# Optimization experiments

Hardware: AMD Instinct MI355X
Metric: run time of the kernel (lower is better)

Reference implementation:

```python
import jax, jax.numpy as jnp
import numpy as np

D_MODEL = 768
HEADS = 12
D_K = D_MODEL // HEADS
NEG = -1e9


def setup_inputs() -> dict:
    key = jax.random.key(0)
    ks = jax.random.split(key, 7)
    B, S, D = 4, 2048, D_MODEL
    scale = 1.0 / np.sqrt(D)
    q = jax.random.normal(ks[0], (B, S, D), dtype=jnp.float32)
    k = jax.random.normal(ks[1], (B, S, D), dtype=jnp.float32)
    v = jax.random.normal(ks[2], (B, S, D), dtype=jnp.float32)
    # causal mask, broadcastable over batch and heads; mask==0 -> -1e9
    mask = jnp.tril(jnp.ones((1, 1, S, S), dtype=jnp.int32))
    W_q = jax.random.normal(ks[3], (D, D), dtype=jnp.float32) * scale
    W_k = jax.random.normal(ks[4], (D, D), dtype=jnp.float32) * scale
    W_v = jax.random.normal(ks[5], (D, D), dtype=jnp.float32) * scale
    W_o = jax.random.normal(ks[6], (D, D), dtype=jnp.float32) * scale
    return {"q": q, "k": k, "v": v, "mask": mask,
            "W_q": W_q, "W_k": W_k, "W_v": W_v, "W_o": W_o}


def reference(q, k, v, mask, W_q, W_k, W_v, W_o):
    B, S, D = q.shape
    # nn.Linear(bias=False): y = x @ W.T
    query = (q @ W_q.T).reshape(B, S, HEADS, D_K).transpose(0, 2, 1, 3)  # [B,H,S,dk]
    key_ = (k @ W_k.T).reshape(B, S, HEADS, D_K).transpose(0, 2, 1, 3)
    value = (v @ W_v.T).reshape(B, S, HEADS, D_K).transpose(0, 2, 1, 3)
    scores = jnp.einsum('bhqd,bhkd->bhqk', query, key_) / jnp.sqrt(
        jnp.asarray(D_K, dtype=query.dtype))
    scores = jnp.where(mask == 0, jnp.asarray(NEG, dtype=scores.dtype), scores)
    attn = jax.nn.softmax(scores, axis=-1)
    # dropout rate = 0.0 (inference / eval mode): identity
    x = jnp.einsum('bhqk,bhkd->bhqd', attn, value)  # [B,H,S,dk]
    x = x.transpose(0, 2, 1, 3).reshape(B, S, D)
    return x @ W_o.T
```

## Files before the change

kernel.cpp:

```cpp
#include <hip/hip_runtime.h>


typedef _Float16 f16x8 __attribute__((ext_vector_type(8)));
typedef _Float16 f16x4 __attribute__((ext_vector_type(4)));
typedef float floatx4 __attribute__((ext_vector_type(4)));

#define MFMA16(a, b, c) __builtin_amdgcn_mfma_f32_16x16x32_f16((a), (b), (c), 0, 0, 0)

static constexpr int B_ = 4;
static constexpr int S_ = 2048;
static constexpr int D_ = 768;
static constexpr int H_ = 12;
static constexpr int DK = 64;

__device__ __forceinline__ f16x8 cvt8(float4 a, float4 b) {
  f16x8 h;
  h[0] = (_Float16)a.x; h[1] = (_Float16)a.y;
  h[2] = (_Float16)a.z; h[3] = (_Float16)a.w;
  h[4] = (_Float16)b.x; h[5] = (_Float16)b.y;
  h[6] = (_Float16)b.z; h[7] = (_Float16)b.w;
  return h;
}

__device__ __forceinline__ void dma16(const _Float16* g, _Float16* l) {
  __builtin_amdgcn_global_load_lds(
      (const __attribute__((address_space(1))) unsigned int*)g,
      (__attribute__((address_space(3))) unsigned int*)l, 16, 0, 0);
}

struct CvtArgs {
  const float* src[7];
  _Float16* dst[7];
  int end[7];
  int nseg;
};

__global__ __launch_bounds__(256) void cvt_f32_f16(CvtArgs a) {
  int b = blockIdx.x;
  int s = 0;
  while (s < a.nseg - 1 && b >= a.end[s]) ++s;
  int local = b - (s ? a.end[s - 1] : 0);
  const int tid = threadIdx.x;
  const float4* p = (const float4*)(a.src[s] + (size_t)local * 2048) + tid * 2;
  float4 x0 = p[0], x1 = p[1];
  *(f16x8*)(a.dst[s] + (size_t)local * 2048 + tid * 8) = cvt8(x0, x1);
}

static constexpr int PAN = 128 * 32;

struct QkvPtrs {
  const void* a[3];
  const void* w[3];
};

template <int MODE, bool SCALE>
__device__ __forceinline__ void gemm_core64(const _Float16* __restrict__ A,
                                            const _Float16* __restrict__ Bm,
                                            void* __restrict__ Cv,
                                            _Float16* As, _Float16* Bs,
                                            int m0, int n0, int N, int K) {
  const int tid = threadIdx.x;
  const int wave = tid >> 6, lane = tid & 63;
  const int l15 = lane & 15, quad = lane >> 4;
  const int wm = (wave >> 1) * 64, wn = (wave & 1) * 64;
  const int lr = lane >> 2;
  const int lc = (lane & 3) * 8;
  const int wb = wave * 16;

  floatx4 acc[4][4] = {};

  for (int k0 = 0; k0 < K; k0 += 64) {
    {
      const _Float16* g = A + (size_t)(m0 + wb + lr) * K + k0 + lc;
      dma16(g, As + wb * 32);
      dma16(g + 32, As + PAN + wb * 32);
      const _Float16* g2 = g + (size_t)64 * K;
      dma16(g2, As + (64 + wb) * 32);
      dma16(g2 + 32, As + PAN + (64 + wb) * 32);
    }
    {
      const _Float16* g = Bm + (size_t)(n0 + wb + lr) * K + k0 + lc;
      dma16(g, Bs + wb * 32);
      dma16(g + 32, Bs + PAN + wb * 32);
      const _Float16* g2 = g + (size_t)64 * K;
      dma16(g2, Bs + (64 + wb) * 32);
      dma16(g2 + 32, Bs + PAN + (64 + wb) * 32);
    }
    __syncthreads();

#pragma unroll
    for (int p = 0; p < 2; ++p) {
      f16x8 af[4], bf[4];
#pragma unroll
      for (int t = 0; t < 4; ++t)
        af[t] = *(const f16x8*)(As + p * PAN + (wm + t * 16 + l15) * 32 +
                                quad * 8);
#pragma unroll
      for (int t = 0; t < 4; ++t)
        bf[t] = *(const f16x8*)(Bs + p * PAN + (wn + t * 16 + l15) * 32 +
                                quad * 8);
#pragma unroll
      for (int mt = 0; mt < 4; ++mt)
#pragma unroll
        for (int nt = 0; nt < 4; ++nt)
          acc[mt][nt] = MFMA16(af[mt], bf[nt], acc[mt][nt]);
    }
    __syncthreads();
  }

  if constexpr (MODE == 2) {
#pragma unroll
    for (int mt = 0; mt < 4; ++mt)
#pragma unroll
      for (int nt = 0; nt < 4; ++nt) {
        int row = m0 + wm + mt * 16 + quad * 4;
        int col = n0 + wn + nt * 16 + l15;
        int b = row >> 11, s = row & 2047;
        int h = col >> 6, d = col & 63;
        f16x4 v4;
#pragma unroll
        for (int r = 0; r < 4; ++r) v4[r] = (_Float16)acc[mt][nt][r];
        *(f16x4*)((_Float16*)Cv + ((size_t)(b * H_ + h) * DK + d) * S_ + s) =
            v4;
      }
  } else {
#pragma unroll
    for (int mt = 0; mt < 4; ++mt)
#pragma unroll
      for (int nt = 0; nt < 4; ++nt)
#pragma unroll
        for (int r = 0; r < 4; ++r) {
          int row = m0 + wm + mt * 16 + quad * 4 + r;
          int col = n0 + wn + nt * 16 + l15;
          float val = acc[mt][nt][r];
          if constexpr (SCALE) val *= 0.125f;
          if constexpr (MODE == 0) {
            ((float*)Cv)[(size_t)row * N + col] = val;
          } else {
            int b = row >> 11, s = row & 2047;
            int h = col >> 6, d = col & 63;
            ((_Float16*)Cv)[((size_t)(b * H_ + h) * S_ + s) * DK + d] =
                (_Float16)val;
          }
        }
  }
}

__global__ __launch_bounds__(256) void qkv_gemm64(QkvPtrs P, _Float16* Qh,
                                                  _Float16* Kh, _Float16* Vt) {
  __shared__ _Float16 As[2 * PAN];
  __shared__ _Float16 Bs[2 * PAN];
  const int linear =
      blockIdx.x + gridDim.x * (blockIdx.y + gridDim.y * blockIdx.z);
  const int xcd = linear & 7;
  const int idx = linear >> 3;
  const int z = idx / 48;
  const int r = idx % 48;
  const int mp = xcd * 8 + (r / 6);
  const int n = r % 6;
  const int m0 = mp * 128, n0 = n * 128;
  if (z == 0) {
    gemm_core64<1, true>((const _Float16*)P.a[0], (const _Float16*)P.w[0], Qh,
                         As, Bs, m0, n0, D_, D_);
  } else if (z == 1) {
    gemm_core64<1, false>((const _Float16*)P.a[1], (const _Float16*)P.w[1], Kh,
                          As, Bs, m0, n0, D_, D_);
  } else {
    gemm_core64<2, false>((const _Float16*)P.a[2], (const _Float16*)P.w[2], Vt,
                          As, Bs, m0, n0, D_, D_);
  }
}

static constexpr int PAN_A = 64 * 32;
static constexpr int PAN_B = 128 * 32;

__global__ __launch_bounds__(256) void gemm_o64(const _Float16* __restrict__ A,
                                                const _Float16* __restrict__ W,
                                                float* __restrict__ C) {
  __shared__ _Float16 As[2 * PAN_A];
  __shared__ _Float16 Bs[2 * PAN_B];
  constexpr int K = 768, N = 768;

  const int linear = blockIdx.x + gridDim.x * blockIdx.y;
  const int xcd = linear & 7;
  const int idx = linear >> 3;
  const int mp = xcd * 16 + idx / 6;
  const int n = idx % 6;
  const int m0 = mp * 64, n0 = n * 128;

  const int tid = threadIdx.x;
  const int wave = tid >> 6, lane = tid & 63;
  const int l15 = lane & 15, quad = lane >> 4;
  const int wm = (wave >> 1) * 32, wn = (wave & 1) * 64;
  const int lr = lane >> 2, lc = (lane & 3) * 8;

  floatx4 acc[2][4] = {};

  for (int k0 = 0; k0 < K; k0 += 64) {
#pragma unroll
    for (int p = 0; p < 2; ++p) {
      const _Float16* g =
          A + (size_t)(m0 + wave * 16 + lr) * K + k0 + p * 32 + lc;
      dma16(g, As + p * PAN_A + wave * 16 * 32);
    }
#pragma unroll
    for (int p = 0; p < 2; ++p)
#pragma unroll
      for (int q = 0; q < 2; ++q) {
        const _Float16* g =
            W + (size_t)(n0 + wave * 32 + q * 16 + lr) * K + k0 + p * 32 + lc;
        dma16(g, Bs + p * PAN_B + (wave * 32 + q * 16) * 32);
      }
    __syncthreads();

#pragma unroll
    for (int p = 0; p < 2; ++p) {
      f16x8 af[2], bf[4];
#pragma unroll
      for (int t = 0; t < 2; ++t)
        af[t] = *(const f16x8*)(As + p * PAN_A + (wm + t * 16 + l15) * 32 +
                                quad * 8);
#pragma unroll
      for (int t = 0; t < 4; ++t)
        bf[t] = *(const f16x8*)(Bs + p * PAN_B + (wn + t * 16 + l15) * 32 +
                                quad * 8);
#pragma unroll
      for (int mt = 0; mt < 2; ++mt)
#pragma unroll
        for (int nt = 0; nt < 4; ++nt)
          acc[mt][nt] = MFMA16(af[mt], bf[nt], acc[mt][nt]);
    }
    __syncthreads();
  }

#pragma unroll
  for (int mt = 0; mt < 2; ++mt)
#pragma unroll
    for (int nt = 0; nt < 4; ++nt)
#pragma unroll
      for (int r = 0; r < 4; ++r) {
        int row = m0 + wm + mt * 16 + quad * 4 + r;
        int col = n0 + wn + nt * 16 + l15;
        C[(size_t)row * N + col] = acc[mt][nt][r];
      }
}

__global__ __launch_bounds__(256, 4) void flash_attn(
    const _Float16* __restrict__ Qh, const _Float16* __restrict__ Kh,
    const _Float16* __restrict__ Vt, _Float16* __restrict__ Oh) {
  __shared__ _Float16 Ks[64 * 72];
  __shared__ _Float16 Vts[64 * 72];
  __shared__ _Float16 Ps[4][16 * 36];

  const int tid = threadIdx.x;
  const int wave = tid >> 6, lane = tid & 63;
  const int l15 = lane & 15, quad = lane >> 4;

  const int linear = blockIdx.x + gridDim.x * blockIdx.y;
  const int xcd = linear & 7;
  const int seq = linear >> 3;
  const int bh = xcd * 6 + (seq >> 4);
  const int xp = seq & 15;
  const int b = bh / H_, h = bh % H_;
  const size_t base = (size_t)bh * S_ * DK;
  const size_t basev = (size_t)bh * DK * S_;

  const int srow = tid >> 2;
  const int sc0 = (tid & 3) * 16;

  for (int c = 0; c < 2; ++c) {
    const int qt = c ? xp : 31 - xp;
    const int q0 = qt * 64;
    const int qrow = q0 + wave * 16 + l15;
    f16x8 qf0 = *(const f16x8*)(Qh + base + (size_t)qrow * DK + quad * 8);
    f16x8 qf1 = *(const f16x8*)(Qh + base + (size_t)qrow * DK + 32 + quad * 8);

    floatx4 o_acc[4] = {};
    float plsum[4] = {0.f, 0.f, 0.f, 0.f};

    const _Float16* ks = Kh + base + (size_t)srow * DK + sc0;
    const _Float16* vs = Vt + basev + (size_t)srow * S_ + sc0;
    f16x8 pk0 = *(const f16x8*)ks;
    f16x8 pk1 = *(const f16x8*)(ks + 8);
    f16x8 pv0 = *(const f16x8*)vs;
    f16x8 pv1 = *(const f16x8*)(vs + 8);

    for (int j = 0; j <= qt; ++j) {
      __syncthreads();
      *(f16x8*)(Ks + srow * 72 + sc0) = pk0;
      *(f16x8*)(Ks + srow * 72 + sc0 + 8) = pk1;
      *(f16x8*)(Vts + srow * 72 + sc0) = pv0;
      *(f16x8*)(Vts + srow * 72 + sc0 + 8) = pv1;
      __syncthreads();

      if (j < qt) {
        const _Float16* kn =
            Kh + base + (size_t)((j + 1) * 64 + srow) * DK + sc0;
        const _Float16* vn =
            Vt + basev + (size_t)srow * S_ + (j + 1) * 64 + sc0;
        pk0 = *(const f16x8*)kn;
        pk1 = *(const f16x8*)(kn + 8);
        pv0 = *(const f16x8*)vn;
        pv1 = *(const f16x8*)(vn + 8);
      }

      floatx4 s_acc[4] = {};
#pragma unroll
      for (int t = 0; t < 4; ++t) {
        f16x8 kf0 = *(const f16x8*)(Ks + (t * 16 + l15) * 72 + quad * 8);
        f16x8 kf1 = *(const f16x8*)(Ks + (t * 16 + l15) * 72 + 32 + quad * 8);
        s_acc[t] = MFMA16(qf0, kf0, s_acc[t]);
        s_acc[t] = MFMA16(qf1, kf1, s_acc[t]);
      }

      const bool diag = (j == qt);
      const int j0 = j * 64;
      float p[4][4];
#pragma unroll
      for (int t = 0; t < 4; ++t)
#pragma unroll
        for (int r = 0; r < 4; ++r) {
          float s = s_acc[t][r];
          if (diag) {
            int rg = q0 + wave * 16 + quad * 4 + r;
            int cg = j0 + t * 16 + l15;
            if (cg > rg) s = -1e30f;
          }
          float e = __expf(s);
          p[t][r] = e;
          plsum[r] += e;
        }

#pragma unroll
      for (int t = 0; t < 2; ++t)
#pragma unroll
        for (int r = 0; r < 4; ++r)
          Ps[wave][(quad * 4 + r) * 36 + t * 16 + l15] = (_Float16)p[t][r];
      f16x8 pf0 = *(const f16x8*)(Ps[wave] + l15 * 36 + quad * 8);
#pragma unroll
      for (int t = 0; t < 4; ++t) {
        f16x8 vf0 = *(const f16x8*)(Vts + (t * 16 + l15) * 72 + quad * 8);
        o_acc[t] = MFMA16(pf0, vf0, o_acc[t]);
      }
#pragma unroll
      for (int t = 2; t < 4; ++t)
#pragma unroll
        for (int r = 0; r < 4; ++r)
          Ps[wave][(quad * 4 + r) * 36 + (t - 2) * 16 + l15] =
              (_Float16)p[t][r];
      f16x8 pf1 = *(const f16x8*)(Ps[wave] + l15 * 36 + quad * 8);
#pragma unroll
      for (int t = 0; t < 4; ++t) {
        f16x8 vf1 = *(const f16x8*)(Vts + (t * 16 + l15) * 72 + 32 + quad * 8);
        o_acc[t] = MFMA16(pf1, vf1, o_acc[t]);
      }
    }

#pragma unroll
    for (int r = 0; r < 4; ++r) {
      float l = plsum[r];
      l += __shfl_xor(l, 1);
      l += __shfl_xor(l, 2);
      l += __shfl_xor(l, 4);
      l += __shfl_xor(l, 8);
      float inv = 1.0f / l;
      int row = q0 + wave * 16 + quad * 4 + r;
#pragma unroll
      for (int t = 0; t < 4; ++t) {
        float val = o_acc[t][r] * inv;
        Oh[((size_t)(b * S_ + row)) * D_ + h * DK + t * 16 + l15] =
            (_Float16)val;
      }
    }
  }
}

template <int MODE, bool SCALE>
__global__ __launch_bounds__(256) void gemm128(const float* __restrict__ Av,
                                               const float* __restrict__ Bv,
                                               void* __restrict__ Cv, int M,
                                               int N, int K) {
  __shared__ _Float16 As[128 * 40];
  __shared__ _Float16 Bs[128 * 40];

  const int tid = threadIdx.x;
  const int wave = tid >> 6, lane = tid & 63;
  const int l15 = lane & 15, quad = lane >> 4;
  const int wm = (wave >> 1) * 64, wn = (wave & 1) * 64;
  const int m0 = blockIdx.y * 128, n0 = blockIdx.x * 128;
  const int srow = tid >> 1, scol = (tid & 1) * 16;

  floatx4 acc[4][4] = {};

  for (int k0 = 0; k0 < K; k0 += 32) {
    {
      const float4* p =
          (const float4*)(Av + (size_t)(m0 + srow) * K + k0 + scol);
      float4 x0 = p[0], x1 = p[1], x2 = p[2], x3 = p[3];
      *(f16x8*)(As + srow * 40 + scol) = cvt8(x0, x1);
      *(f16x8*)(As + srow * 40 + scol + 8) = cvt8(x2, x3);
    }
    {
      const float4* p =
          (const float4*)(Bv + (size_t)(n0 + srow) * K + k0 + scol);
      float4 x0 = p[0], x1 = p[1], x2 = p[2], x3 = p[3];
      *(f16x8*)(Bs + srow * 40 + scol) = cvt8(x0, x1);
      *(f16x8*)(Bs + srow * 40 + scol + 8) = cvt8(x2, x3);
    }
    __syncthreads();

    f16x8 af[4], bf[4];
#pragma unroll
    for (int t = 0; t < 4; ++t)
      af[t] = *(const f16x8*)(As + (wm + t * 16 + l15) * 40 + quad * 8);
#pragma unroll
    for (int t = 0; t < 4; ++t)
      bf[t] = *(const f16x8*)(Bs + (wn + t * 16 + l15) * 40 + quad * 8);
#pragma unroll
    for (int mt = 0; mt < 4; ++mt)
#pragma unroll
      for (int nt = 0; nt < 4; ++nt)
        acc[mt][nt] = MFMA16(af[mt], bf[nt], acc[mt][nt]);
    __syncthreads();
  }

#pragma unroll
  for (int mt = 0; mt < 4; ++mt)
#pragma unroll
    for (int nt = 0; nt < 4; ++nt)
#pragma unroll
      for (int r = 0; r < 4; ++r) {
        int row = m0 + wm + mt * 16 + quad * 4 + r;
        int col = n0 + wn + nt * 16 + l15;
        float val = acc[mt][nt][r];
        if constexpr (SCALE) val *= 0.125f;
        if constexpr (MODE == 0) {
          ((float*)Cv)[(size_t)row * N + col] = val;
        } else if constexpr (MODE == 1) {
          int b = row >> 11, s = row & 2047;
          int h = col >> 6, d = col & 63;
          ((_Float16*)Cv)[((size_t)(b * H_ + h) * S_ + s) * DK + d] =
              (_Float16)val;
        } else {
          int b = col >> 11, s = col & 2047;
          int h = row >> 6, d = row & 63;
          ((_Float16*)Cv)[((size_t)(b * H_ + h) * DK + d) * S_ + s] =
              (_Float16)val;
        }
      }
}

__global__ __launch_bounds__(256) void gemm_out_f32w(
    const _Float16* __restrict__ A, const float* __restrict__ Bv,
    float* __restrict__ C) {
  __shared__ _Float16 As[128 * 40];
  __shared__ _Float16 Bs[128 * 40];
  constexpr int K = 768, N = 768;

  const int tid = threadIdx.x;
  const int wave = tid >> 6, lane = tid & 63;
  const int l15 = lane & 15, quad = lane >> 4;
  const int wm = (wave >> 1) * 64, wn = (wave & 1) * 64;
  const int m0 = blockIdx.y * 128, n0 = blockIdx.x * 128;
  const int srow = tid >> 1, scol = (tid & 1) * 16;

  floatx4 acc[4][4] = {};

  for (int k0 = 0; k0 < K; k0 += 32) {
    {
      const f16x8* p = (const f16x8*)(A + (size_t)(m0 + srow) * K + k0 + scol);
      *(f16x8*)(As + srow * 40 + scol) = p[0];
      *(f16x8*)(As + srow * 40 + scol + 8) = p[1];
    }
    {
      const float4* p =
          (const float4*)(Bv + (size_t)(n0 + srow) * K + k0 + scol);
      float4 x0 = p[0], x1 = p[1], x2 = p[2], x3 = p[3];
      *(f16x8*)(Bs + srow * 40 + scol) = cvt8(x0, x1);
      *(f16x8*)(Bs + srow * 40 + scol + 8) = cvt8(x2, x3);
    }
    __syncthreads();

    f16x8 af[4], bf[4];
#pragma unroll
    for (int t = 0; t < 4; ++t)
      af[t] = *(const f16x8*)(As + (wm + t * 16 + l15) * 40 + quad * 8);
#pragma unroll
    for (int t = 0; t < 4; ++t)
      bf[t] = *(const f16x8*)(Bs + (wn + t * 16 + l15) * 40 + quad * 8);
#pragma unroll
    for (int mt = 0; mt < 4; ++mt)
#pragma unroll
      for (int nt = 0; nt < 4; ++nt)
        acc[mt][nt] = MFMA16(af[mt], bf[nt], acc[mt][nt]);
    __syncthreads();
  }

#pragma unroll
  for (int mt = 0; mt < 4; ++mt)
#pragma unroll
    for (int nt = 0; nt < 4; ++nt)
#pragma unroll
      for (int r = 0; r < 4; ++r) {
        int row = m0 + wm + mt * 16 + quad * 4 + r;
        int col = n0 + wn + nt * 16 + l15;
        C[(size_t)row * N + col] = acc[mt][nt][r];
      }
}

extern "C" void kernel_launch(void* const* d_in, const int* in_sizes, int n_in,
                              void* d_out, int out_size, void* d_ws,
                              size_t ws_size, hipStream_t stream) {
  const float* q = (const float*)d_in[0];
  const float* k = (const float*)d_in[1];
  const float* v = (const float*)d_in[2];
  const float* Wq = (const float*)d_in[4];
  const float* Wk = (const float*)d_in[5];
  const float* Wv = (const float*)d_in[6];
  const float* Wo = (const float*)d_in[7];
  float* out = (float*)d_out;

  const size_t E = (size_t)B_ * H_ * S_ * DK;
  const size_t EW = (size_t)D_ * D_;
  _Float16* Qh = (_Float16*)d_ws;
  _Float16* Kh = Qh + E;
  _Float16* Vt = Kh + E;
  _Float16* Oh = Vt + E;

  const int M = B_ * S_;
  dim3 blk(256);
  dim3 qg(D_ / 128, M / 128, 3);
  dim3 og(D_ / 128, M / 64);
  dim3 pg(D_ / 128, M / 128);
  dim3 fg(16, B_ * H_);

  const size_t need_full = (7 * E + 4 * EW) * 2;

  if (ws_size >= need_full) {
    _Float16* qf = Oh + E;
    _Float16* kf = qf + E;
    _Float16* vf = kf + E;
    _Float16* wqf = vf + E;
    _Float16* wkf = wqf + EW;
    _Float16* wvf = wkf + EW;
    _Float16* wof = wvf + EW;
    CvtArgs ca;
    ca.src[0] = q;  ca.dst[0] = qf;
    ca.src[1] = k;  ca.dst[1] = kf;
    ca.src[2] = v;  ca.dst[2] = vf;
    ca.src[3] = Wq; ca.dst[3] = wqf;
    ca.src[4] = Wk; ca.dst[4] = wkf;
    ca.src[5] = Wv; ca.dst[5] = wvf;
    ca.src[6] = Wo; ca.dst[6] = wof;
    int ends[7] = {3072, 6144, 9216, 9504, 9792, 10080, 10368};
    for (int i = 0; i < 7; ++i) ca.end[i] = ends[i];
    ca.nseg = 7;
    cvt_f32_f16<<<10368, blk, 0, stream>>>(ca);
    QkvPtrs P;
    P.a[0] = qf; P.a[1] = kf; P.a[2] = vf;
    P.w[0] = wqf; P.w[1] = wkf; P.w[2] = wvf;
    qkv_gemm64<<<qg, blk, 0, stream>>>(P, Qh, Kh, Vt);
    flash_attn<<<fg, blk, 0, stream>>>(Qh, Kh, Vt, Oh);
    gemm_o64<<<og, blk, 0, stream>>>(Oh, wof, out);
  } else {
    gemm128<1, true><<<pg, blk, 0, stream>>>(q, Wq, Qh, M, D_, D_);
    gemm128<1, false><<<pg, blk, 0, stream>>>(k, Wk, Kh, M, D_, D_);
    gemm128<2, false><<<dim3(M / 128, D_ / 128), blk, 0, stream>>>(
        Wv, v, Vt, D_, M, D_);
    flash_attn<<<fg, blk, 0, stream>>>(Qh, Kh, Vt, Oh);
    gemm_out_f32w<<<pg, blk, 0, stream>>>(Oh, Wo, out);
  }
}
```

Baseline: 245.5 us.

## Rework flash attention to 32x32 MFMA tiles with key-split waves

The attention kernel moves from 16x16x32 MFMA tiles to 32x32x16 tiles. The four waves are reorganised into two row halves times two key halves, and each loop iteration stages a 128-key K/V tile. The two key-half partial outputs and row sums are combined through shared memory at the end. The goal is fewer MFMA issues and fewer LDS fragment reads per FLOP. In exchange the kernel uses more registers and LDS, is limited to 3 blocks per SM, adds extra syncs, and causal masking leaves some key-half waves idle.

```diff
diff --git a/kernel.cpp b/kernel.cpp
--- a/kernel.cpp
+++ b/kernel.cpp
@@ -4,8 +4,10 @@
 typedef _Float16 f16x8 __attribute__((ext_vector_type(8)));
 typedef _Float16 f16x4 __attribute__((ext_vector_type(4)));
 typedef float floatx4 __attribute__((ext_vector_type(4)));
+typedef float floatx16 __attribute__((ext_vector_type(16)));
 
 #define MFMA16(a, b, c) __builtin_amdgcn_mfma_f32_16x16x32_f16((a), (b), (c), 0, 0, 0)
+#define MFMA32(a, b, c) __builtin_amdgcn_mfma_f32_32x32x16_f16((a), (b), (c), 0, 0, 0)
 
 static constexpr int B_ = 4;
 static constexpr int S_ = 2048;
@@ -245,16 +247,17 @@
       }
 }
 
-__global__ __launch_bounds__(256, 4) void flash_attn(
+__global__ __launch_bounds__(256, 3) void flash_attn(
     const _Float16* __restrict__ Qh, const _Float16* __restrict__ Kh,
     const _Float16* __restrict__ Vt, _Float16* __restrict__ Oh) {
-  __shared__ _Float16 Ks[64 * 72];
-  __shared__ _Float16 Vts[64 * 72];
-  __shared__ _Float16 Ps[4][16 * 36];
+  __shared__ _Float16 Ks[128 * 72];
+  __shared__ _Float16 Vts[64 * 136];
+  __shared__ _Float16 Ps[4][32 * 36];
 
   const int tid = threadIdx.x;
   const int wave = tid >> 6, lane = tid & 63;
-  const int l15 = lane & 15, quad = lane >> 4;
+  const int l31 = lane & 31, sub = lane >> 5;
+  const int rowhalf = wave & 1, keyhalf = wave >> 1;
 
   const int linear = blockIdx.x + gridDim.x * blockIdx.y;
   const int xcd = linear & 7;
@@ -266,112 +269,148 @@
   const size_t basev = (size_t)bh * DK * S_;
 
   const int srow = tid >> 2;
-  const int sc0 = (tid & 3) * 16;
+  const int scol = (tid & 3) * 16;
+  const int vcol = (tid & 3) * 32;
 
   for (int c = 0; c < 2; ++c) {
     const int qt = c ? xp : 31 - xp;
     const int q0 = qt * 64;
-    const int qrow = q0 + wave * 16 + l15;
-    f16x8 qf0 = *(const f16x8*)(Qh + base + (size_t)qrow * DK + quad * 8);
-    f16x8 qf1 = *(const f16x8*)(Qh + base + (size_t)qrow * DK + 32 + quad * 8);
-
-    floatx4 o_acc[4] = {};
-    float plsum[4] = {0.f, 0.f, 0.f, 0.f};
-
-    const _Float16* ks = Kh + base + (size_t)srow * DK + sc0;
-    const _Float16* vs = Vt + basev + (size_t)srow * S_ + sc0;
-    f16x8 pk0 = *(const f16x8*)ks;
-    f16x8 pk1 = *(const f16x8*)(ks + 8);
-    f16x8 pv0 = *(const f16x8*)vs;
-    f16x8 pv1 = *(const f16x8*)(vs + 8);
-
-    for (int j = 0; j <= qt; ++j) {
+    const int nt = qt + 1;
+    const int iters = (nt + 1) >> 1;
+    const int rbase = q0 + rowhalf * 32;
+
+    f16x8 qf[4];
+#pragma unroll
+    for (int ks = 0; ks < 4; ++ks)
+      qf[ks] = *(const f16x8*)(Qh + base + (size_t)(rbase + l31) * DK +
+                               ks * 16 + sub * 8);
+
+    floatx16 o0 = {}, o1 = {};
+    float plsum[16] = {};
+
+    f16x8 pk[4], pv[4];
+    {
+      const _Float16* kp = Kh + base + (size_t)srow * DK + scol;
+      pk[0] = *(const f16x8*)kp;
+      pk[1] = *(const f16x8*)(kp + 8);
+      const _Float16* kp2 = kp + (size_t)64 * DK;
+      pk[2] = *(const f16x8*)kp2;
+      pk[3] = *(const f16x8*)(kp2 + 8);
+      const _Float16* vp = Vt + basev + (size_t)srow * S_ + vcol;
+#pragma unroll
+      for (int j = 0; j < 4; ++j) pv[j] = *(const f16x8*)(vp + j * 8);
+    }
+
+    for (int i = 0; i < iters; ++i) {
       __syncthreads();
-      *(f16x8*)(Ks + srow * 72 + sc0) = pk0;
-      *(f16x8*)(Ks + srow * 72 + sc0 + 8) = pk1;
-      *(f16x8*)(Vts + srow * 72 + sc0) = pv0;
-      *(f16x8*)(Vts + srow * 72 + sc0 + 8) = pv1;
+      *(f16x8*)(Ks + srow * 72 + scol) = pk[0];
+      *(f16x8*)(Ks + srow * 72 + scol + 8) = pk[1];
+      *(f16x8*)(Ks + (64 + srow) * 72 + scol) = pk[2];
+      *(f16x8*)(Ks + (64 + srow) * 72 + scol + 8) = pk[3];
+#pragma unroll
+      for (int j = 0; j < 4; ++j)
+        *(f16x8*)(Vts + srow * 136 + vcol + j * 8) = pv[j];
       __syncthreads();
 
-      if (j < qt) {
-        const _Float16* kn =
-            Kh + base + (size_t)((j + 1) * 64 + srow) * DK + sc0;
-        const _Float16* vn =
-            Vt + basev + (size_t)srow * S_ + (j + 1) * 64 + sc0;
-        pk0 = *(const f16x8*)kn;
-        pk1 = *(const f16x8*)(kn + 8);
-        pv0 = *(const f16x8*)vn;
-        pv1 = *(const f16x8*)(vn + 8);
-      }
-
-      floatx4 s_acc[4] = {};
-#pragma unroll
-      for (int t = 0; t < 4; ++t) {
-        f16x8 kf0 = *(const f16x8*)(Ks + (t * 16 + l15) * 72 + quad * 8);
-        f16x8 kf1 = *(const f16x8*)(Ks + (t * 16 + l15) * 72 + 32 + quad * 8);
-        s_acc[t] = MFMA16(qf0, kf0, s_acc[t]);
-        s_acc[t] = MFMA16(qf1, kf1, s_acc[t]);
-      }
-
-      const bool diag = (j == qt);
-      const int j0 = j * 64;
-      float p[4][4];
-#pragma unroll
-      for (int t = 0; t < 4; ++t)
-#pragma unroll
-        for (int r = 0; r < 4; ++r) {
-          float s = s_acc[t][r];
-          if (diag) {
-            int rg = q0 + wave * 16 + quad * 4 + r;
-            int cg = j0 + t * 16 + l15;
+      if (i + 1 < iters) {
+        const int g0 = (i + 1) * 128;
+        const _Float16* kp = Kh + base + (size_t)(g0 + srow) * DK + scol;
+        pk[0] = *(const f16x8*)kp;
+        pk[1] = *(const f16x8*)(kp + 8);
+        const _Float16* kp2 = kp + (size_t)64 * DK;
+        pk[2] = *(const f16x8*)kp2;
+        pk[3] = *(const f16x8*)(kp2 + 8);
+        const _Float16* vp = Vt + basev + (size_t)srow * S_ + g0 + vcol;
+#pragma unroll
+        for (int j = 0; j < 4; ++j) pv[j] = *(const f16x8*)(vp + j * 8);
+      }
+
+      const int kb = i * 128 + keyhalf * 64;
+      if (kb > rbase + 31) continue;
+
+      floatx16 s0 = {}, s1 = {};
+#pragma unroll
+      for (int ks = 0; ks < 4; ++ks) {
+        f16x8 kf0 = *(const f16x8*)(Ks + (keyhalf * 64 + l31) * 72 + ks * 16 +
+                                    sub * 8);
+        f16x8 kf1 = *(const f16x8*)(Ks + (keyhalf * 64 + 32 + l31) * 72 +
+                                    ks * 16 + sub * 8);
+        s0 = MFMA32(qf[ks], kf0, s0);
+        s1 = MFMA32(qf[ks], kf1, s1);
+      }
+
+#pragma unroll
+      for (int t = 0; t < 2; ++t) {
+        floatx16 sv = t ? s1 : s0;
+        const int cg = kb + t * 32 + l31;
+        const bool nm = (kb + t * 32 + 31 > rbase);
+#pragma unroll
+        for (int reg = 0; reg < 16; ++reg) {
+          float s = sv[reg];
+          if (nm) {
+            int rg = rbase + (reg & 3) + 8 * (reg >> 2) + 4 * sub;
             if (cg > rg) s = -1e30f;
           }
           float e = __expf(s);
-          p[t][r] = e;
-          plsum[r] += e;
+          plsum[reg] += e;
+          Ps[wave][((reg & 3) + 8 * (reg >> 2) + 4 * sub) * 36 + l31] =
+              (_Float16)e;
         }
-
-#pragma unroll
-      for (int t = 0; t < 2; ++t)
-#pragma unroll
-        for (int r = 0; r < 4; ++r)
-          Ps[wave][(quad * 4 + r) * 36 + t * 16 + l15] = (_Float16)p[t][r];
-      f16x8 pf0 = *(const f16x8*)(Ps[wave] + l15 * 36 + quad * 8);
-#pragma unroll
-      for (int t = 0; t < 4; ++t) {
-        f16x8 vf0 = *(const f16x8*)(Vts + (t * 16 + l15) * 72 + quad * 8);
-        o_acc[t] = MFMA16(pf0, vf0, o_acc[t]);
-      }
-#pragma unroll
-      for (int t = 2; t < 4; ++t)
-#pragma unroll
-        for (int r = 0; r < 4; ++r)
-          Ps[wave][(quad * 4 + r) * 36 + (t - 2) * 16 + l15] =
-              (_Float16)p[t][r];
-      f16x8 pf1 = *(const f16x8*)(Ps[wave] + l15 * 36 + quad * 8);
-#pragma unroll
-      for (int t = 0; t < 4; ++t) {
-        f16x8 vf1 = *(const f16x8*)(Vts + (t * 16 + l15) * 72 + 32 + quad * 8);
-        o_acc[t] = MFMA16(pf1, vf1, o_acc[t]);
-      }
-    }
-
-#pragma unroll
-    for (int r = 0; r < 4; ++r) {
-      float l = plsum[r];
+        f16x8 pf0 = *(const f16x8*)(Ps[wave] + l31 * 36 + sub * 8);
+        f16x8 pf1 = *(const f16x8*)(Ps[wave] + l31 * 36 + 16 + sub * 8);
+        const int kk = keyhalf * 64 + t * 32;
+        f16x8 va0 = *(const f16x8*)(Vts + l31 * 136 + kk + sub * 8);
+        f16x8 va1 = *(const f16x8*)(Vts + l31 * 136 + kk + 16 + sub * 8);
+        f16x8 vb0 = *(const f16x8*)(Vts + (32 + l31) * 136 + kk + sub * 8);
+        f16x8 vb1 = *(const f16x8*)(Vts + (32 + l31) * 136 + kk + 16 + sub * 8);
+        o0 = MFMA32(pf0, va0, o0);
+        o0 = MFMA32(pf1, va1, o0);
+        o1 = MFMA32(pf0, vb0, o1);
+        o1 = MFMA32(pf1, vb1, o1);
+      }
+    }
+
+#pragma unroll
+    for (int reg = 0; reg < 16; ++reg) {
+      float l = plsum[reg];
       l += __shfl_xor(l, 1);
       l += __shfl_xor(l, 2);
       l += __shfl_xor(l, 4);
       l += __shfl_xor(l, 8);
-      float inv = 1.0f / l;
-      int row = q0 + wave * 16 + quad * 4 + r;
-#pragma unroll
-      for (int t = 0; t < 4; ++t) {
-        float val = o_acc[t][r] * inv;
-        Oh[((size_t)(b * S_ + row)) * D_ + h * DK + t * 16 + l15] =
-            (_Float16)val;
-      }
-    }
+      l += __shfl_xor(l, 16);
+      plsum[reg] = l;
+    }
+
+    float* fb = (float*)Ks;
+    float* lb = (float*)Vts;
+    __syncthreads();
+    if (keyhalf == 1) {
+      float* d0 = fb + rowhalf * 2048 + lane * 32;
+#pragma unroll
+      for (int reg = 0; reg < 16; ++reg) {
+        d0[reg] = o0[reg];
+        d0[16 + reg] = o1[reg];
+      }
+      float* dl = lb + rowhalf * 1024 + lane * 16;
+#pragma unroll
+      for (int reg = 0; reg < 16; ++reg) dl[reg] = plsum[reg];
+    }
+    __syncthreads();
+    if (keyhalf == 0) {
+      const float* s0p = fb + rowhalf * 2048 + lane * 32;
+      const float* slp = lb + rowhalf * 1024 + lane * 16;
+#pragma unroll
+      for (int reg = 0; reg < 16; ++reg) {
+        float inv = 1.0f / (plsum[reg] + slp[reg]);
+        int row = rbase + (reg & 3) + 8 * (reg >> 2) + 4 * sub;
+        float v0 = (o0[reg] + s0p[reg]) * inv;
+        float v1 = (o1[reg] + s0p[16 + reg]) * inv;
+        _Float16* op = Oh + ((size_t)(b * S_ + row)) * D_ + h * DK;
+        op[l31] = (_Float16)v0;
+        op[32 + l31] = (_Float16)v1;
+      }
+    }
+    __syncthreads();
   }
 }
 
```

New measurement: 299.7 us. 1.22x slower.
